# Optimization experiments

Hardware: AMD Instinct MI355X
Metric: run time of the kernel (lower is better)

## Reference

```python
import jax, jax.numpy as jnp
import numpy as np

N, DIM, C = 100000, 512, 2
D = DIM // 2


def setup_inputs() -> dict:
    key = jax.random.key(0)
    ks = jax.random.split(key, 13)
    s_dim = 1.0 / np.sqrt(DIM)
    s_d = 1.0 / np.sqrt(D)
    return {
        "h": jax.random.normal(ks[0], (N, DIM), dtype=jnp.float32),
        # adaptor: Linear(dim, dim//2) -> ReLU -> Linear(dim//2, dim)
        "W1": jax.random.uniform(ks[1], (D, DIM), jnp.float32, -s_dim, s_dim),
        "b1": jax.random.uniform(ks[2], (D,), jnp.float32, -s_dim, s_dim),
        "W2": jax.random.uniform(ks[3], (DIM, D), jnp.float32, -s_d, s_d),
        "b2": jax.random.uniform(ks[4], (DIM,), jnp.float32, -s_d, s_d),
        # per-class gated attention nets, stacked over class dim C
        "Wa": jax.random.uniform(ks[5], (C, D, DIM), jnp.float32, -s_dim, s_dim),
        "ba": jax.random.uniform(ks[6], (C, D), jnp.float32, -s_dim, s_dim),
        "Wb": jax.random.uniform(ks[7], (C, D, DIM), jnp.float32, -s_dim, s_dim),
        "bb": jax.random.uniform(ks[8], (C, D), jnp.float32, -s_dim, s_dim),
        "Wc": jax.random.uniform(ks[9], (C, D), jnp.float32, -s_d, s_d),
        "bc": jax.random.uniform(ks[10], (C,), jnp.float32, -s_d, s_d),
        # per-class classifiers Linear(dim, 1)
        "Wclf": jax.random.uniform(ks[11], (C, DIM), jnp.float32, -s_dim, s_dim),
        "bclf": jax.random.uniform(ks[12], (C,), jnp.float32, -s_dim, s_dim),
    }


def reference(h, W1, b1, W2, b2, Wa, ba, Wb, bb, Wc, bc, Wclf, bclf):
    # residual adaptor: h = h + Linear2(relu(Linear1(h)))
    hid = jax.nn.relu(h @ W1.T + b1)          # [N, D]
    h = h + hid @ W2.T + b2                   # [N, DIM]

    # gated attention, vectorized over classes: a*b -> Linear(D, 1)
    a = jnp.tanh(jnp.einsum('nd,ckd->cnk', h, Wa) + ba[:, None, :])      # [C, N, D]
    g = jax.nn.sigmoid(jnp.einsum('nd,ckd->cnk', h, Wb) + bb[:, None, :])
    A_logits = jnp.einsum('cnk,ck->cn', a * g, Wc) + bc[:, None]         # [C, N]

    A = jax.nn.softmax(A_logits, axis=1)       # softmax over instances, [C, N]
    M = jnp.einsum('cn,nd->cd', A, h)          # pooled bag features, [C, DIM]
    logits = (jnp.einsum('cd,cd->c', M, Wclf) + bclf)[None, :]           # [1, C]

    Y_prob = jax.nn.softmax(logits, axis=1)
    Y_hat = jnp.argmax(logits, axis=1, keepdims=True)
    features = M[-1:]                          # torch loop keeps last class's M
    return (logits, Y_prob, Y_hat, A, features)
```

## Files before the change

kernel.cpp:

```cpp
#include <hip/hip_runtime.h>
#include <math.h>

#define N_ROWS 100000
#define DIM    512
#define DHID   256
#define NCLS   2
#define BN     32
#define NCHUNK 64

typedef _Float16 f16;
typedef __attribute__((ext_vector_type(8))) _Float16 f16x8;
typedef __attribute__((ext_vector_type(4))) _Float16 f16x4;
typedef __attribute__((ext_vector_type(2))) _Float16 f16x2;
typedef __attribute__((ext_vector_type(4))) float f32x4;

__device__ inline float frcp(float x){
#if __has_builtin(__builtin_amdgcn_rcpf)
    return __builtin_amdgcn_rcpf(x);
#else
    return 1.f / x;
#endif
}

__device__ __forceinline__ void gll16(const f16* g, f16* l) {
    __builtin_amdgcn_global_load_lds(
        (const __attribute__((address_space(1))) void*)g,
        (__attribute__((address_space(3))) void*)l, 16, 0, 0);
}

__global__ __launch_bounds__(256)
void k0_cvt(const float* __restrict__ W1, const float* __restrict__ W2,
            const float* __restrict__ Wa, const float* __restrict__ Wb,
            f16* __restrict__ out)
{
    int i = (blockIdx.x * 256 + threadIdx.x) * 4;
    const float* src; int off;
    if      (i < 131072) { src = W1; off = 0; }
    else if (i < 262144) { src = W2; off = 131072; }
    else if (i < 524288) { src = Wa; off = 262144; }
    else                 { src = Wb; off = 524288; }
    float4 v = *(const float4*)(src + (i - off));
    f16x4 o; o[0] = (f16)v.x; o[1] = (f16)v.y; o[2] = (f16)v.z; o[3] = (f16)v.w;
    *(f16x4*)(out + i) = o;
}

#define MFMA(a,b,c) __builtin_amdgcn_mfma_f32_16x16x32_f16((a),(b),(c),0,0,0)

__global__ __launch_bounds__(512, 4)
void k1_fused(const float* __restrict__ h,
              const f16* __restrict__ W1f, const float* __restrict__ b1,
              const f16* __restrict__ W2f, const float* __restrict__ b2,
              const f16* __restrict__ Waf, const float* __restrict__ ba,
              const f16* __restrict__ Wbf, const float* __restrict__ bb,
              const float* __restrict__ Wc, const float* __restrict__ bc,
              f16* __restrict__ hnew16, float* __restrict__ A_logits)
{
    __shared__ __align__(16) f16 sh_h[BN * DIM];
    __shared__ __align__(16) f16 sh_hid[BN * DHID];
    __shared__ __align__(16) f16 sh_wb[16384];

    const int tid  = threadIdx.x;
    const int lane = tid & 63;
    const int w    = tid >> 6;
    const int l16  = lane & 15;
    const int grp  = lane >> 4;
    const int n0   = blockIdx.x * BN;

    #define SWZH(row, col) ((row) * DIM  + ((col) ^ (((row) & 7) << 3)))
    #define SWZD(row, col) ((row) * DHID + ((col) ^ (((row) & 7) << 3)))

    #define STAGE_B(P, KROW, kb, bufbase)                                     \
    do {                                                                      \
        int u0 = tid;                                                         \
        int c0_ = u0 >> 2, ks0 = (u0 & 3) ^ ((u0 >> 3) & 3);                  \
        gll16((P) + (size_t)c0_ * (KROW) + (kb) + ks0 * 8,                    \
              &sh_wb[(bufbase) + u0 * 8]);                                    \
        int u1 = tid + 512;                                                   \
        int c1_ = u1 >> 2, ks1 = (u1 & 3) ^ ((u1 >> 3) & 3);                  \
        gll16((P) + (size_t)c1_ * (KROW) + (kb) + ks1 * 8,                    \
              &sh_wb[(bufbase) + u1 * 8]);                                    \
    } while (0)

    const int bslot = grp ^ ((l16 >> 1) & 3);
    #define BFRAG(bufbase, T) \
        (*(const f16x8*)&sh_wb[(bufbase) + (((T) * 16 + l16) * 4 + bslot) * 8])

    {
        const float4* hsrc = (const float4*)(h + (size_t)n0 * DIM);
        #pragma unroll
        for (int i = 0; i < 4; ++i) {
            int c = tid + 512 * i;
            int row = c >> 6, colb = (c & 63) * 8;
            float4 lo = hsrc[c * 2], hi = hsrc[c * 2 + 1];
            f16x8 v;
            v[0] = (f16)lo.x; v[1] = (f16)lo.y; v[2] = (f16)lo.z; v[3] = (f16)lo.w;
            v[4] = (f16)hi.x; v[5] = (f16)hi.y; v[6] = (f16)hi.z; v[7] = (f16)hi.w;
            *(f16x8*)&sh_h[SWZH(row, colb)] = v;
        }
    }
    STAGE_B(W1f, DIM, 0, 0);
    __syncthreads();

    {
        f32x4 c00 = {0,0,0,0}, c01 = {0,0,0,0}, c10 = {0,0,0,0}, c11 = {0,0,0,0};
        #pragma unroll
        for (int kt = 0; kt < 16; ++kt) {
            const int bb = (kt & 1) * 8192;
            if (kt < 15) STAGE_B(W1f, DIM, (kt + 1) * 32, ((kt + 1) & 1) * 8192);
            int kc = kt * 32 + grp * 8;
            f16x8 a0 = *(const f16x8*)&sh_h[SWZH(l16,      kc)];
            f16x8 a1 = *(const f16x8*)&sh_h[SWZH(16 + l16, kc)];
            f16x8 b0 = BFRAG(bb, w);
            f16x8 b1v = BFRAG(bb, w + 8);
            c00 = MFMA(a0, b0, c00);  c10 = MFMA(a1, b0, c10);
            c01 = MFMA(a0, b1v, c01); c11 = MFMA(a1, b1v, c11);
            __syncthreads();
        }
        STAGE_B(W2f, DHID, 0, 0);
        #pragma unroll
        for (int q = 0; q < 2; ++q) {
            int col = (w + 8 * q) * 16 + l16;
            float bias = b1[col];
            f32x4 cm0 = q ? c01 : c00, cm1 = q ? c11 : c10;
            #pragma unroll
            for (int j = 0; j < 4; ++j) {
                int r0 = grp * 4 + j;
                float v0 = cm0[j] + bias; v0 = v0 > 0.f ? v0 : 0.f;
                float v1 = cm1[j] + bias; v1 = v1 > 0.f ? v1 : 0.f;
                sh_hid[SWZD(r0,      col)] = (f16)v0;
                sh_hid[SWZD(16 + r0, col)] = (f16)v1;
            }
        }
        __syncthreads();
    }

    #pragma unroll
    for (int half = 0; half < 2; ++half) {
        const f16* P = W2f + (size_t)half * 256 * DHID;
        f32x4 acc[2][2];
        #pragma unroll
        for (int m = 0; m < 2; ++m)
            #pragma unroll
            for (int q = 0; q < 2; ++q) acc[m][q] = (f32x4){0,0,0,0};
        #pragma unroll
        for (int kt = 0; kt < 8; ++kt) {
            const int bb = (kt & 1) * 8192;
            if (kt < 7) STAGE_B(P, DHID, (kt + 1) * 32, ((kt + 1) & 1) * 8192);
            int kc = kt * 32 + grp * 8;
            f16x8 a0 = *(const f16x8*)&sh_hid[SWZD(l16,      kc)];
            f16x8 a1 = *(const f16x8*)&sh_hid[SWZD(16 + l16, kc)];
            f16x8 b0 = BFRAG(bb, w);
            f16x8 b1v = BFRAG(bb, w + 8);
            acc[0][0] = MFMA(a0, b0, acc[0][0]);  acc[1][0] = MFMA(a1, b0, acc[1][0]);
            acc[0][1] = MFMA(a0, b1v, acc[0][1]); acc[1][1] = MFMA(a1, b1v, acc[1][1]);
            __syncthreads();
        }
        if (half == 0) STAGE_B(W2f + (size_t)256 * DHID, DHID, 0, 0);
        else           STAGE_B(Waf, DIM, 0, 0);
        #pragma unroll
        for (int q = 0; q < 2; ++q) {
            int col = half * 256 + (w + 8 * q) * 16 + l16;
            float bias = b2[col];
            #pragma unroll
            for (int m = 0; m < 2; ++m)
                #pragma unroll
                for (int j = 0; j < 4; ++j) {
                    int row = m * 16 + grp * 4 + j;
                    int so  = SWZH(row, col);
                    float v = acc[m][q][j] + bias + (float)sh_h[so];
                    f16 hv = (f16)v;
                    sh_h[so] = hv;
                    hnew16[(size_t)(n0 + row) * DIM + col] = hv;
                }
        }
        __syncthreads();
    }

    float* sh_redf = (float*)&sh_wb[8192];
    for (int c = 0; c < NCLS; ++c) {
        f32x4 aA[2][2], aG[2][2];
        #pragma unroll
        for (int m = 0; m < 2; ++m)
            #pragma unroll
            for (int q = 0; q < 2; ++q) { aA[m][q] = (f32x4){0,0,0,0}; aG[m][q] = (f32x4){0,0,0,0}; }

        const f16* PA = Waf + (size_t)c * DHID * DIM;
        const f16* PB = Wbf + (size_t)c * DHID * DIM;
        #pragma unroll
        for (int kt = 0; kt < 16; ++kt) {
            const int bb = (kt & 1) * 8192;
            if (kt < 15) STAGE_B(PA, DIM, (kt + 1) * 32, ((kt + 1) & 1) * 8192);
            int kc = kt * 32 + grp * 8;
            f16x8 a0 = *(const f16x8*)&sh_h[SWZH(l16,      kc)];
            f16x8 a1 = *(const f16x8*)&sh_h[SWZH(16 + l16, kc)];
            f16x8 b0 = BFRAG(bb, w);
            f16x8 b1v = BFRAG(bb, w + 8);
            aA[0][0] = MFMA(a0, b0, aA[0][0]);  aA[1][0] = MFMA(a1, b0, aA[1][0]);
            aA[0][1] = MFMA(a0, b1v, aA[0][1]); aA[1][1] = MFMA(a1, b1v, aA[1][1]);
            __syncthreads();
        }
        STAGE_B(PB, DIM, 0, 0);
        __syncthreads();
        #pragma unroll
        for (int kt = 0; kt < 16; ++kt) {
            const int bb = (kt & 1) * 8192;
            if (kt < 15) STAGE_B(PB, DIM, (kt + 1) * 32, ((kt + 1) & 1) * 8192);
            int kc = kt * 32 + grp * 8;
            f16x8 a0 = *(const f16x8*)&sh_h[SWZH(l16,      kc)];
            f16x8 a1 = *(const f16x8*)&sh_h[SWZH(16 + l16, kc)];
            f16x8 b0 = BFRAG(bb, w);
            f16x8 b1v = BFRAG(bb, w + 8);
            aG[0][0] = MFMA(a0, b0, aG[0][0]);  aG[1][0] = MFMA(a1, b0, aG[1][0]);
            aG[0][1] = MFMA(a0, b1v, aG[0][1]); aG[1][1] = MFMA(a1, b1v, aG[1][1]);
            __syncthreads();
        }
        float vsum[2][4];
        #pragma unroll
        for (int m = 0; m < 2; ++m)
            #pragma unroll
            for (int j = 0; j < 4; ++j) vsum[m][j] = 0.f;
        #pragma unroll
        for (int q = 0; q < 2; ++q) {
            int col = (w + 8 * q) * 16 + l16;
            float bav = ba[c * DHID + col];
            float bbv = bb[c * DHID + col];
            float wcv = Wc[c * DHID + col];
            #pragma unroll
            for (int m = 0; m < 2; ++m)
                #pragma unroll
                for (int j = 0; j < 4; ++j) {
                    float sa = aA[m][q][j] + bav;
                    float sg = aG[m][q][j] + bbv;
                    float ea = __expf(2.f * sa);
                    float ta = 1.f - 2.f * frcp(ea + 1.f);
                    float sgm = frcp(1.f + __expf(-sg));
                    vsum[m][j] += ta * sgm * wcv;
                }
        }
        #pragma unroll
        for (int m = 0; m < 2; ++m)
            #pragma unroll
            for (int j = 0; j < 4; ++j) {
                float v = vsum[m][j];
                v += __shfl_xor(v, 1); v += __shfl_xor(v, 2);
                v += __shfl_xor(v, 4); v += __shfl_xor(v, 8);
                if (l16 == 0) sh_redf[w * BN + m * 16 + grp * 4 + j] = v;
            }
        __syncthreads();
        if (tid < BN) {
            float s = bc[c];
            #pragma unroll
            for (int ww = 0; ww < 8; ++ww) s += sh_redf[ww * BN + tid];
            A_logits[(size_t)c * N_ROWS + n0 + tid] = s;
        }
        __syncthreads();
        if (c == 0) { STAGE_B(Waf + (size_t)DHID * DIM, DIM, 0, 0); __syncthreads(); }
    }
    #undef SWZH
    #undef SWZD
    #undef STAGE_B
    #undef BFRAG
}

__global__ __launch_bounds__(256)
void k2a_partial(const float* __restrict__ A_logits, float2* __restrict__ partials)
{
    const int c     = blockIdx.x >> 6;
    const int chunk = blockIdx.x & 63;
    const int per   = (N_ROWS + NCHUNK - 1) / NCHUNK;
    const int i0 = chunk * per;
    const int i1 = min(i0 + per, N_ROWS);
    const int tid = threadIdx.x, lane = tid & 63, w = tid >> 6;
    const float* L = A_logits + (size_t)c * N_ROWS;
    __shared__ float sm[4], ss[4];

    float m = -1e30f;
    for (int i = i0 + tid; i < i1; i += 256) m = fmaxf(m, L[i]);
    #pragma unroll
    for (int o = 1; o < 64; o <<= 1) m = fmaxf(m, __shfl_xor(m, o));
    if (lane == 0) sm[w] = m;
    __syncthreads();
    m = fmaxf(fmaxf(sm[0], sm[1]), fmaxf(sm[2], sm[3]));

    float s = 0.f;
    for (int i = i0 + tid; i < i1; i += 256) s += __expf(L[i] - m);
    #pragma unroll
    for (int o = 1; o < 64; o <<= 1) s += __shfl_xor(s, o);
    if (lane == 0) ss[w] = s;
    __syncthreads();
    if (tid == 0) {
        float2 p; p.x = m; p.y = ss[0] + ss[1] + ss[2] + ss[3];
        partials[blockIdx.x] = p;
    }
}

__global__ __launch_bounds__(256)
void k2b_combine(const float2* __restrict__ partials, float2* __restrict__ MS,
                 float* __restrict__ Mbuf)
{
    const int tid = threadIdx.x;
    #pragma unroll
    for (int i = 0; i < 4; ++i) Mbuf[tid + 256 * i] = 0.f;
    if (tid < 128) {
        const int c = tid >> 6, lane = tid & 63;
        float2 p = partials[c * 64 + lane];
        float M = p.x;
        #pragma unroll
        for (int o = 1; o < 64; o <<= 1) M = fmaxf(M, __shfl_xor(M, o));
        float s = p.y * __expf(p.x - M);
        #pragma unroll
        for (int o = 1; o < 64; o <<= 1) s += __shfl_xor(s, o);
        if (lane == 0) { float2 r; r.x = M; r.y = 1.f / s; MS[c] = r; }
    }
}

__global__ __launch_bounds__(256)
void k3_pool(const float* __restrict__ A_logits, const float2* __restrict__ MS,
             const f16* __restrict__ hnew16, float* __restrict__ A_out,
             float* __restrict__ Mbuf)
{
    const int tid = threadIdx.x, lane = tid & 63, w = tid >> 6;
    const int per = (N_ROWS + gridDim.x - 1) / gridDim.x;
    const int r0 = blockIdx.x * per;
    const int r1 = min(r0 + per, N_ROWS);
    const float2 ms0 = MS[0], ms1 = MS[1];
    __shared__ float red[4][2][DIM];

    float acc0[8], acc1[8];
    #pragma unroll
    for (int j = 0; j < 8; ++j) { acc0[j] = 0.f; acc1[j] = 0.f; }

    for (int n = r0 + w; n < r1; n += 4) {
        float w0 = __expf(A_logits[n]          - ms0.x) * ms0.y;
        float w1 = __expf(A_logits[N_ROWS + n] - ms1.x) * ms1.y;
        if (lane == 0)      A_out[n] = w0;
        else if (lane == 1) A_out[N_ROWS + n] = w1;
        f16x8 hv = *(const f16x8*)(hnew16 + (size_t)n * DIM + lane * 8);
        #pragma unroll
        for (int j = 0; j < 8; ++j) {
            float hx = (float)hv[j];
            acc0[j] += w0 * hx;
            acc1[j] += w1 * hx;
        }
    }
    #pragma unroll
    for (int j = 0; j < 8; ++j) {
        red[w][0][lane * 8 + j] = acc0[j];
        red[w][1][lane * 8 + j] = acc1[j];
    }
    __syncthreads();
    #pragma unroll
    for (int t = 0; t < 4; ++t) {
        int idx = tid + t * 256;
        int c = idx >> 9, d = idx & 511;
        float s = red[0][c][d] + red[1][c][d] + red[2][c][d] + red[3][c][d];
        atomicAdd(&Mbuf[c * DIM + d], s);
    }
}

__global__ __launch_bounds__(512)
void k4_final(const float* __restrict__ Mbuf,
              const float* __restrict__ Wclf, const float* __restrict__ bclf,
              float* __restrict__ out)
{
    __shared__ float red[16];
    const int tid  = threadIdx.x;
    const int lane = tid & 63;
    const int wid  = tid >> 6;

    float m0 = Mbuf[tid];
    float m1 = Mbuf[DIM + tid];
    float p0 = m0 * Wclf[tid];
    float p1 = m1 * Wclf[DIM + tid];
    #pragma unroll
    for (int o = 1; o < 64; o <<= 1) {
        p0 += __shfl_xor(p0, o);
        p1 += __shfl_xor(p1, o);
    }
    if (lane == 0) { red[wid] = p0; red[8 + wid] = p1; }
    __syncthreads();
    if (tid == 0) {
        float l0 = bclf[0], l1 = bclf[1];
        for (int ww = 0; ww < 8; ++ww) { l0 += red[ww]; l1 += red[8 + ww]; }
        out[0] = l0; out[1] = l1;
        float mx = fmaxf(l0, l1);
        float e0 = expf(l0 - mx), e1 = expf(l1 - mx);
        float inv = 1.f / (e0 + e1);
        out[2] = e0 * inv; out[3] = e1 * inv;
        out[4] = (l1 > l0) ? 1.0f : 0.0f;
    }
    out[5 + 2 * N_ROWS + tid] = m1;
}

extern "C" void kernel_launch(void* const* d_in, const int* in_sizes, int n_in,
                              void* d_out, int out_size, void* d_ws, size_t ws_size,
                              hipStream_t stream)
{
    const float* h    = (const float*)d_in[0];
    const float* W1   = (const float*)d_in[1];
    const float* b1   = (const float*)d_in[2];
    const float* W2   = (const float*)d_in[3];
    const float* b2   = (const float*)d_in[4];
    const float* Wa   = (const float*)d_in[5];
    const float* ba   = (const float*)d_in[6];
    const float* Wb   = (const float*)d_in[7];
    const float* bb   = (const float*)d_in[8];
    const float* Wc   = (const float*)d_in[9];
    const float* bc   = (const float*)d_in[10];
    const float* Wclf = (const float*)d_in[11];
    const float* bclf = (const float*)d_in[12];
    float* out = (float*)d_out;

    f16*    hnew16   = (f16*)d_ws;
    f16*    W1f      = (f16*)((char*)d_ws + (size_t)N_ROWS * DIM * 2);
    f16*    W2f      = W1f + 256 * 512;
    f16*    Waf      = W2f + 512 * 256;
    f16*    Wbf      = Waf + 2 * 256 * 512;
    float*  A_logits = (float*)(Wbf + 2 * 256 * 512);
    float*  Mbuf     = A_logits + 2 * (size_t)N_ROWS;
    float2* partials = (float2*)(Mbuf + 1024);
    float2* MS       = partials + 2 * NCHUNK;
    float*  A_out    = out + 5;

    k0_cvt<<<768, 256, 0, stream>>>(W1, W2, Wa, Wb, W1f);
    k1_fused<<<N_ROWS / BN, 512, 0, stream>>>(h, W1f, b1, W2f, b2, Waf, ba,
                                              Wbf, bb, Wc, bc, hnew16, A_logits);
    k2a_partial<<<2 * NCHUNK, 256, 0, stream>>>(A_logits, partials);
    k2b_combine<<<1, 256, 0, stream>>>(partials, MS, Mbuf);
    k3_pool<<<1024, 256, 0, stream>>>(A_logits, MS, hnew16, A_out, Mbuf);
    k4_final<<<1, 512, 0, stream>>>(Mbuf, Wclf, bclf, out);
}
```

Measured before the change: 702.2 us.

## Double row tile to 64 with 2x4 warp grid to halve weight restaging

Raises the fused kernel's row tile from 32 to 64 rows and arranges the 8 warps as a 2x4 grid, so each warp computes 32 rows by 64 columns and every staged weight tile serves twice as many rows. This halves the number of blocks and the total weight traffic through LDS per row. It also issues the next stage's first weight tile prefetch inside the last iteration of each loop, removing the extra barriers between phases. In exchange, shared memory per block grows with the larger h tile and accumulator registers double. Occupancy drops to 2 blocks per CU, and the tail block needs row bounds checks.

```diff
diff --git a/kernel.cpp b/kernel.cpp
--- a/kernel.cpp
+++ b/kernel.cpp
@@ -5,7 +5,7 @@
 #define DIM    512
 #define DHID   256
 #define NCLS   2
-#define BN     32
+#define BN     64
 #define NCHUNK 64
 
 typedef _Float16 f16;
@@ -46,7 +46,7 @@
 
 #define MFMA(a,b,c) __builtin_amdgcn_mfma_f32_16x16x32_f16((a),(b),(c),0,0,0)
 
-__global__ __launch_bounds__(512, 4)
+__global__ __launch_bounds__(512, 2)
 void k1_fused(const float* __restrict__ h,
               const f16* __restrict__ W1f, const float* __restrict__ b1,
               const f16* __restrict__ W2f, const float* __restrict__ b2,
@@ -64,6 +64,8 @@
     const int w    = tid >> 6;
     const int l16  = lane & 15;
     const int grp  = lane >> 4;
+    const int rg   = w >> 2;
+    const int cg   = w & 3;
     const int n0   = blockIdx.x * BN;
 
     #define SWZH(row, col) ((row) * DIM  + ((col) ^ (((row) & 7) << 3)))
@@ -86,12 +88,14 @@
         (*(const f16x8*)&sh_wb[(bufbase) + (((T) * 16 + l16) * 4 + bslot) * 8])
 
     {
-        const float4* hsrc = (const float4*)(h + (size_t)n0 * DIM);
-        #pragma unroll
-        for (int i = 0; i < 4; ++i) {
-            int c = tid + 512 * i;
-            int row = c >> 6, colb = (c & 63) * 8;
-            float4 lo = hsrc[c * 2], hi = hsrc[c * 2 + 1];
+        #pragma unroll
+        for (int i = 0; i < 8; ++i) {
+            int cch = tid + 512 * i;
+            int row = cch >> 6, colb = (cch & 63) * 8;
+            int g = n0 + row;
+            const float4* hsrc = (const float4*)
+                (h + (size_t)(g < N_ROWS ? g : N_ROWS - 1) * DIM + colb);
+            float4 lo = hsrc[0], hi = hsrc[1];
             f16x8 v;
             v[0] = (f16)lo.x; v[1] = (f16)lo.y; v[2] = (f16)lo.z; v[3] = (f16)lo.w;
             v[4] = (f16)hi.x; v[5] = (f16)hi.y; v[6] = (f16)hi.z; v[7] = (f16)hi.w;
@@ -102,75 +106,83 @@
     __syncthreads();
 
     {
-        f32x4 c00 = {0,0,0,0}, c01 = {0,0,0,0}, c10 = {0,0,0,0}, c11 = {0,0,0,0};
+        f32x4 acc[2][4];
+        #pragma unroll
+        for (int m = 0; m < 2; ++m)
+            #pragma unroll
+            for (int q = 0; q < 4; ++q) acc[m][q] = (f32x4){0,0,0,0};
         #pragma unroll
         for (int kt = 0; kt < 16; ++kt) {
             const int bb = (kt & 1) * 8192;
             if (kt < 15) STAGE_B(W1f, DIM, (kt + 1) * 32, ((kt + 1) & 1) * 8192);
+            else         STAGE_B(W2f, DHID, 0, 0);
             int kc = kt * 32 + grp * 8;
-            f16x8 a0 = *(const f16x8*)&sh_h[SWZH(l16,      kc)];
-            f16x8 a1 = *(const f16x8*)&sh_h[SWZH(16 + l16, kc)];
-            f16x8 b0 = BFRAG(bb, w);
-            f16x8 b1v = BFRAG(bb, w + 8);
-            c00 = MFMA(a0, b0, c00);  c10 = MFMA(a1, b0, c10);
-            c01 = MFMA(a0, b1v, c01); c11 = MFMA(a1, b1v, c11);
+            f16x8 a0 = *(const f16x8*)&sh_h[SWZH(rg * 32 + l16,      kc)];
+            f16x8 a1 = *(const f16x8*)&sh_h[SWZH(rg * 32 + 16 + l16, kc)];
+            #pragma unroll
+            for (int q = 0; q < 4; ++q) {
+                f16x8 b = BFRAG(bb, cg * 4 + q);
+                acc[0][q] = MFMA(a0, b, acc[0][q]);
+                acc[1][q] = MFMA(a1, b, acc[1][q]);
+            }
             __syncthreads();
         }
-        STAGE_B(W2f, DHID, 0, 0);
-        #pragma unroll
-        for (int q = 0; q < 2; ++q) {
-            int col = (w + 8 * q) * 16 + l16;
+        #pragma unroll
+        for (int q = 0; q < 4; ++q) {
+            int col = (cg * 4 + q) * 16 + l16;
             float bias = b1[col];
-            f32x4 cm0 = q ? c01 : c00, cm1 = q ? c11 : c10;
-            #pragma unroll
-            for (int j = 0; j < 4; ++j) {
-                int r0 = grp * 4 + j;
-                float v0 = cm0[j] + bias; v0 = v0 > 0.f ? v0 : 0.f;
-                float v1 = cm1[j] + bias; v1 = v1 > 0.f ? v1 : 0.f;
-                sh_hid[SWZD(r0,      col)] = (f16)v0;
-                sh_hid[SWZD(16 + r0, col)] = (f16)v1;
-            }
-        }
-        __syncthreads();
-    }
-
-    #pragma unroll
-    for (int half = 0; half < 2; ++half) {
-        const f16* P = W2f + (size_t)half * 256 * DHID;
-        f32x4 acc[2][2];
-        #pragma unroll
-        for (int m = 0; m < 2; ++m)
-            #pragma unroll
-            for (int q = 0; q < 2; ++q) acc[m][q] = (f32x4){0,0,0,0};
-        #pragma unroll
-        for (int kt = 0; kt < 8; ++kt) {
-            const int bb = (kt & 1) * 8192;
-            if (kt < 7) STAGE_B(P, DHID, (kt + 1) * 32, ((kt + 1) & 1) * 8192);
-            int kc = kt * 32 + grp * 8;
-            f16x8 a0 = *(const f16x8*)&sh_hid[SWZD(l16,      kc)];
-            f16x8 a1 = *(const f16x8*)&sh_hid[SWZD(16 + l16, kc)];
-            f16x8 b0 = BFRAG(bb, w);
-            f16x8 b1v = BFRAG(bb, w + 8);
-            acc[0][0] = MFMA(a0, b0, acc[0][0]);  acc[1][0] = MFMA(a1, b0, acc[1][0]);
-            acc[0][1] = MFMA(a0, b1v, acc[0][1]); acc[1][1] = MFMA(a1, b1v, acc[1][1]);
-            __syncthreads();
-        }
-        if (half == 0) STAGE_B(W2f + (size_t)256 * DHID, DHID, 0, 0);
-        else           STAGE_B(Waf, DIM, 0, 0);
-        #pragma unroll
-        for (int q = 0; q < 2; ++q) {
-            int col = half * 256 + (w + 8 * q) * 16 + l16;
-            float bias = b2[col];
             #pragma unroll
             for (int m = 0; m < 2; ++m)
                 #pragma unroll
                 for (int j = 0; j < 4; ++j) {
-                    int row = m * 16 + grp * 4 + j;
+                    int row = rg * 32 + m * 16 + grp * 4 + j;
+                    float v = acc[m][q][j] + bias;
+                    sh_hid[SWZD(row, col)] = (f16)(v > 0.f ? v : 0.f);
+                }
+        }
+        __syncthreads();
+    }
+
+    #pragma unroll
+    for (int half = 0; half < 2; ++half) {
+        const f16* P = W2f + (size_t)half * 256 * DHID;
+        f32x4 acc[2][4];
+        #pragma unroll
+        for (int m = 0; m < 2; ++m)
+            #pragma unroll
+            for (int q = 0; q < 4; ++q) acc[m][q] = (f32x4){0,0,0,0};
+        #pragma unroll
+        for (int kt = 0; kt < 8; ++kt) {
+            const int bb = (kt & 1) * 8192;
+            if (kt < 7)          STAGE_B(P, DHID, (kt + 1) * 32, ((kt + 1) & 1) * 8192);
+            else if (half == 0)  STAGE_B(W2f + (size_t)256 * DHID, DHID, 0, 0);
+            else                 STAGE_B(Waf, DIM, 0, 0);
+            int kc = kt * 32 + grp * 8;
+            f16x8 a0 = *(const f16x8*)&sh_hid[SWZD(rg * 32 + l16,      kc)];
+            f16x8 a1 = *(const f16x8*)&sh_hid[SWZD(rg * 32 + 16 + l16, kc)];
+            #pragma unroll
+            for (int q = 0; q < 4; ++q) {
+                f16x8 b = BFRAG(bb, cg * 4 + q);
+                acc[0][q] = MFMA(a0, b, acc[0][q]);
+                acc[1][q] = MFMA(a1, b, acc[1][q]);
+            }
+            __syncthreads();
+        }
+        #pragma unroll
+        for (int q = 0; q < 4; ++q) {
+            int col = half * 256 + (cg * 4 + q) * 16 + l16;
+            float bias = b2[col];
+            #pragma unroll
+            for (int m = 0; m < 2; ++m)
+                #pragma unroll
+                for (int j = 0; j < 4; ++j) {
+                    int row = rg * 32 + m * 16 + grp * 4 + j;
                     int so  = SWZH(row, col);
                     float v = acc[m][q][j] + bias + (float)sh_h[so];
                     f16 hv = (f16)v;
                     sh_h[so] = hv;
-                    hnew16[(size_t)(n0 + row) * DIM + col] = hv;
+                    int grow = n0 + row;
+                    if (grow < N_ROWS) hnew16[(size_t)grow * DIM + col] = hv;
                 }
         }
         __syncthreads();
@@ -178,40 +190,44 @@
 
     float* sh_redf = (float*)&sh_wb[8192];
     for (int c = 0; c < NCLS; ++c) {
-        f32x4 aA[2][2], aG[2][2];
-        #pragma unroll
-        for (int m = 0; m < 2; ++m)
-            #pragma unroll
-            for (int q = 0; q < 2; ++q) { aA[m][q] = (f32x4){0,0,0,0}; aG[m][q] = (f32x4){0,0,0,0}; }
-
         const f16* PA = Waf + (size_t)c * DHID * DIM;
         const f16* PB = Wbf + (size_t)c * DHID * DIM;
+        f32x4 aA[2][4], aG[2][4];
+        #pragma unroll
+        for (int m = 0; m < 2; ++m)
+            #pragma unroll
+            for (int q = 0; q < 4; ++q) { aA[m][q] = (f32x4){0,0,0,0}; aG[m][q] = (f32x4){0,0,0,0}; }
+
         #pragma unroll
         for (int kt = 0; kt < 16; ++kt) {
             const int bb = (kt & 1) * 8192;
             if (kt < 15) STAGE_B(PA, DIM, (kt + 1) * 32, ((kt + 1) & 1) * 8192);
+            else         STAGE_B(PB, DIM, 0, 0);
             int kc = kt * 32 + grp * 8;
-            f16x8 a0 = *(const f16x8*)&sh_h[SWZH(l16,      kc)];
-            f16x8 a1 = *(const f16x8*)&sh_h[SWZH(16 + l16, kc)];
-            f16x8 b0 = BFRAG(bb, w);
-            f16x8 b1v = BFRAG(bb, w + 8);
-            aA[0][0] = MFMA(a0, b0, aA[0][0]);  aA[1][0] = MFMA(a1, b0, aA[1][0]);
-            aA[0][1] = MFMA(a0, b1v, aA[0][1]); aA[1][1] = MFMA(a1, b1v, aA[1][1]);
+            f16x8 a0 = *(const f16x8*)&sh_h[SWZH(rg * 32 + l16,      kc)];
+            f16x8 a1 = *(const f16x8*)&sh_h[SWZH(rg * 32 + 16 + l16, kc)];
+            #pragma unroll
+            for (int q = 0; q < 4; ++q) {
+                f16x8 b = BFRAG(bb, cg * 4 + q);
+                aA[0][q] = MFMA(a0, b, aA[0][q]);
+                aA[1][q] = MFMA(a1, b, aA[1][q]);
+            }
             __syncthreads();
         }
-        STAGE_B(PB, DIM, 0, 0);
-        __syncthreads();
         #pragma unroll
         for (int kt = 0; kt < 16; ++kt) {
             const int bb = (kt & 1) * 8192;
-            if (kt < 15) STAGE_B(PB, DIM, (kt + 1) * 32, ((kt + 1) & 1) * 8192);
+            if (kt < 15)      STAGE_B(PB, DIM, (kt + 1) * 32, ((kt + 1) & 1) * 8192);
+            else if (c == 0)  STAGE_B(Waf + (size_t)DHID * DIM, DIM, 0, 0);
             int kc = kt * 32 + grp * 8;
-            f16x8 a0 = *(const f16x8*)&sh_h[SWZH(l16,      kc)];
-            f16x8 a1 = *(const f16x8*)&sh_h[SWZH(16 + l16, kc)];
-            f16x8 b0 = BFRAG(bb, w);
-            f16x8 b1v = BFRAG(bb, w + 8);
-            aG[0][0] = MFMA(a0, b0, aG[0][0]);  aG[1][0] = MFMA(a1, b0, aG[1][0]);
-            aG[0][1] = MFMA(a0, b1v, aG[0][1]); aG[1][1] = MFMA(a1, b1v, aG[1][1]);
+            f16x8 a0 = *(const f16x8*)&sh_h[SWZH(rg * 32 + l16,      kc)];
+            f16x8 a1 = *(const f16x8*)&sh_h[SWZH(rg * 32 + 16 + l16, kc)];
+            #pragma unroll
+            for (int q = 0; q < 4; ++q) {
+                f16x8 b = BFRAG(bb, cg * 4 + q);
+                aG[0][q] = MFMA(a0, b, aG[0][q]);
+                aG[1][q] = MFMA(a1, b, aG[1][q]);
+            }
             __syncthreads();
         }
         float vsum[2][4];
@@ -220,8 +236,8 @@
             #pragma unroll
             for (int j = 0; j < 4; ++j) vsum[m][j] = 0.f;
         #pragma unroll
-        for (int q = 0; q < 2; ++q) {
-            int col = (w + 8 * q) * 16 + l16;
+        for (int q = 0; q < 4; ++q) {
+            int col = (cg * 4 + q) * 16 + l16;
             float bav = ba[c * DHID + col];
             float bbv = bb[c * DHID + col];
             float wcv = Wc[c * DHID + col];
@@ -244,17 +260,19 @@
                 float v = vsum[m][j];
                 v += __shfl_xor(v, 1); v += __shfl_xor(v, 2);
                 v += __shfl_xor(v, 4); v += __shfl_xor(v, 8);
-                if (l16 == 0) sh_redf[w * BN + m * 16 + grp * 4 + j] = v;
+                if (l16 == 0) sh_redf[w * 32 + m * 16 + grp * 4 + j] = v;
             }
         __syncthreads();
         if (tid < BN) {
+            int rg_ = tid >> 5, rloc = tid & 31;
             float s = bc[c];
             #pragma unroll
-            for (int ww = 0; ww < 8; ++ww) s += sh_redf[ww * BN + tid];
-            A_logits[(size_t)c * N_ROWS + n0 + tid] = s;
+            for (int cgi = 0; cgi < 4; ++cgi)
+                s += sh_redf[(rg_ * 4 + cgi) * 32 + rloc];
+            int grow = n0 + tid;
+            if (grow < N_ROWS) A_logits[(size_t)c * N_ROWS + grow] = s;
         }
         __syncthreads();
-        if (c == 0) { STAGE_B(Waf + (size_t)DHID * DIM, DIM, 0, 0); __syncthreads(); }
     }
     #undef SWZH
     #undef SWZD
@@ -423,8 +441,9 @@
     float*  A_out    = out + 5;
 
     k0_cvt<<<768, 256, 0, stream>>>(W1, W2, Wa, Wb, W1f);
-    k1_fused<<<N_ROWS / BN, 512, 0, stream>>>(h, W1f, b1, W2f, b2, Waf, ba,
-                                              Wbf, bb, Wc, bc, hnew16, A_logits);
+    k1_fused<<<(N_ROWS + BN - 1) / BN, 512, 0, stream>>>(h, W1f, b1, W2f, b2,
+                                              Waf, ba, Wbf, bb, Wc, bc,
+                                              hnew16, A_logits);
     k2a_partial<<<2 * NCHUNK, 256, 0, stream>>>(A_logits, partials);
     k2b_combine<<<1, 256, 0, stream>>>(partials, MS, Mbuf);
     k3_pool<<<1024, 256, 0, stream>>>(A_logits, MS, hnew16, A_out, Mbuf);
```

Measured after the change: 689.9 us. About the same (-1.8%).
